# Optimization experiments

Measured on AMD Instinct MI355X. Metric: run time of the kernel, lower is better.

Reference implementation:

```python
import jax, jax.numpy as jnp
import numpy as np

N_NODES = 50000
NEG_SLOPE = 0.2


def _gat_layer(x, src, dst, W, att_src, att_dst, bias, concat):
    # x: [N, F_in]; W: [F_in, H*D]; att_*: [H, D]; bias: [H*D] or [D]
    H, D = att_src.shape
    N = x.shape[0]
    h = (x @ W).reshape(N, H, D)                       # [N, H, D]
    a_s = jnp.einsum('nhd,hd->nh', h, att_src)         # [N, H]
    a_d = jnp.einsum('nhd,hd->nh', h, att_dst)
    e = a_s[src] + a_d[dst]                            # [E, H]
    e = jnp.where(e > 0, e, NEG_SLOPE * e)             # LeakyReLU(0.2)
    # segment softmax over incoming edges of each target node
    e_max = jax.ops.segment_max(e, dst, num_segments=N)
    ex = jnp.exp(e - e_max[dst])
    denom = jax.ops.segment_sum(ex, dst, num_segments=N)
    alpha = ex / denom[dst]                            # [E, H]
    msg = h[src] * alpha[:, :, None]                   # [E, H, D]
    out = jax.ops.segment_sum(msg, dst, num_segments=N)  # [N, H, D]
    if concat:
        out = out.reshape(N, H * D)
    else:
        out = out.mean(axis=1)
    return out + bias


def _forward(x, edge_index, W1, att_src1, att_dst1, b1, W2, att_src2, att_dst2, b2):
    N = x.shape[0]
    loop = jnp.arange(N, dtype=edge_index.dtype)
    src = jnp.concatenate([edge_index[0], loop])       # add self-loops (PyG default)
    dst = jnp.concatenate([edge_index[1], loop])
    h = _gat_layer(x, src, dst, W1, att_src1, att_dst1, b1, concat=True)
    h = jax.nn.elu(h)
    h = _gat_layer(h, src, dst, W2, att_src2, att_dst2, b2, concat=False)
    return jax.nn.log_softmax(h, axis=-1)


def setup_inputs() -> dict:
    key = jax.random.key(0)
    ks = jax.random.split(key, 12)
    N, E, F_in, F_out, H, D = N_NODES, 1600000, 128, 64, 8, 32
    glorot = lambda k, shp: jax.random.normal(k, shp, jnp.float32) * np.sqrt(2.0 / (shp[0] + shp[-1]))
    return {
        'x': jax.random.normal(ks[0], (N, F_in), jnp.float32),
        'edge_index': jax.random.randint(ks[1], (2, E), 0, N, jnp.int64),
        'W1': glorot(ks[2], (F_in, H * D)),
        'att_src1': glorot(ks[3], (H, D)),
        'att_dst1': glorot(ks[4], (H, D)),
        'b1': jnp.zeros((H * D,), jnp.float32),
        'W2': glorot(ks[5], (H * D, F_out)),
        'att_src2': glorot(ks[6], (1, F_out)),
        'att_dst2': glorot(ks[7], (1, F_out)),
        'b2': jnp.zeros((F_out,), jnp.float32),
    }


def reference(x, edge_index, W1, att_src1, att_dst1, b1, W2, att_src2, att_dst2, b2):
    return _forward(x, edge_index, W1, att_src1, att_dst1, b1, W2, att_src2, att_dst2, b2)
```

## Files before the change

### kernel.cpp

```cpp
#include <hip/hip_runtime.h>
#include <hip/hip_bf16.h>
#include <math.h>


#define FIN 128
#define C1 256
#define NH 8
#define HD 32
#define C2 64
#define CH1 64

typedef float floatx2 __attribute__((ext_vector_type(2)));
typedef short bf16x8 __attribute__((ext_vector_type(8)));
typedef float f32x4 __attribute__((ext_vector_type(4)));

__device__ __forceinline__ float blo(unsigned u) { return __uint_as_float(u << 16); }
__device__ __forceinline__ float bhi(unsigned u) { return __uint_as_float(u & 0xffff0000u); }
__device__ __forceinline__ unsigned pkbf(float a, float b) {
    unsigned ua = __float_as_uint(a), ub = __float_as_uint(b);
    ua += 0x7fff + ((ua >> 16) & 1);
    ub += 0x7fff + ((ub >> 16) & 1);
    return (ua >> 16) | (ub & 0xffff0000u);
}

__global__ void init_kernel(const float* __restrict__ W1, const float* __restrict__ W2,
                            int* __restrict__ cnt, unsigned short* __restrict__ w1t,
                            unsigned short* __restrict__ w2t, int n) {
    int i = blockIdx.x * 256 + threadIdx.x;
    if (i < n) cnt[i] = 1;
    if (i < C1 * FIN) {
        int j = i >> 7, k = i & 127;
        float v = W1[(size_t)k * C1 + j];
        w1t[i] = (unsigned short)(pkbf(v, v) & 0xffffu);
    } else if (i < C1 * FIN + C2 * C1) {
        int j2 = i - C1 * FIN;
        int j = j2 >> 8, k = j2 & 255;
        float v = W2[(size_t)k * C2 + j];
        w2t[j2] = (unsigned short)(pkbf(v, v) & 0xffffu);
    }
}

__global__ void hist_kernel(const int* __restrict__ ei, int E, int T,
                            int* cnt, int* __restrict__ offs) {
    int base = blockIdx.x * 256 + threadIdx.x;
    if (base >= T) return;
    int d[4], o[4];
    #pragma unroll
    for (int i = 0; i < 4; ++i) {
        int e = base + i * T;
        d[i] = (e < E) ? ei[E + e] : -1;
    }
    #pragma unroll
    for (int i = 0; i < 4; ++i)
        if (d[i] >= 0) o[i] = atomicAdd(&cnt[d[i]], 1);
    #pragma unroll
    for (int i = 0; i < 4; ++i)
        if (d[i] >= 0) offs[base + i * T] = o[i];
}

__global__ void scan1_kernel(const int* __restrict__ cnt, int n,
                             int* __restrict__ pref, int* __restrict__ bsum) {
    int tid = threadIdx.x, lane = tid & 63, w = tid >> 6;
    int i = blockIdx.x * 256 + tid;
    int v = (i < n) ? cnt[i] : 0;
    int sc = v;
    #pragma unroll
    for (int d = 1; d < 64; d <<= 1) {
        int t = __shfl_up(sc, d, 64);
        if (lane >= d) sc += t;
    }
    __shared__ int ws[4];
    if (lane == 63) ws[w] = sc;
    __syncthreads();
    int woff = 0;
    #pragma unroll
    for (int k = 0; k < 4; ++k) woff += (k < w) ? ws[k] : 0;
    if (i < n) pref[i] = woff + sc - v;
    if (tid == 255) bsum[blockIdx.x] = woff + sc;
}

__global__ void scan2_kernel(int* bsum, int nb) {
    int tid = threadIdx.x, lane = tid & 63, w = tid >> 6;
    int v = (tid < nb) ? bsum[tid] : 0;
    int sc = v;
    #pragma unroll
    for (int d = 1; d < 64; d <<= 1) {
        int t = __shfl_up(sc, d, 64);
        if (lane >= d) sc += t;
    }
    __shared__ int ws[4];
    if (lane == 63) ws[w] = sc;
    __syncthreads();
    int woff = 0;
    #pragma unroll
    for (int k = 0; k < 4; ++k) woff += (k < w) ? ws[k] : 0;
    __syncthreads();
    if (tid < nb) bsum[tid] = woff + sc - v;
}

__global__ void scan3_kernel(const int* __restrict__ pref, const int* __restrict__ bsum,
                             int n, int ETOT, int* __restrict__ rowptr,
                             int* __restrict__ colb) {
    int i = blockIdx.x * 256 + threadIdx.x;
    if (i < n) {
        int rp = pref[i] + bsum[blockIdx.x];
        rowptr[i] = rp;
        colb[rp] = i;
    }
    if (i == 0) rowptr[n] = ETOT;
}

__global__ __launch_bounds__(256) void gemm1_scatter_fused(
    const float* __restrict__ x, const unsigned short* __restrict__ w1t,
    const float* __restrict__ att_s, const float* __restrict__ att_d,
    unsigned char* __restrict__ h1, float* __restrict__ as1, float* __restrict__ ad1,
    int Nn, int GB1,
    const int* __restrict__ ei, const int* __restrict__ rowptr,
    const int* __restrict__ offs, int E, int T, int* __restrict__ colb) {
    __shared__ __align__(16) unsigned char sA[64 * 256];
    int tid = threadIdx.x;
    if (blockIdx.x >= GB1) {
        int base = (blockIdx.x - GB1) * 256 + tid;
        if (base >= T) return;
        #pragma unroll
        for (int i = 0; i < 4; ++i) {
            int e = base + i * T;
            if (e >= E) continue;
            int src = ei[e], dst = ei[E + e];
            colb[rowptr[dst] + offs[e]] = src;
        }
        return;
    }
    int row0 = blockIdx.x * 64;
    #pragma unroll
    for (int rep = 0; rep < 4; ++rep) {
        int flat = rep * 256 + tid;
        int row = flat >> 4, c16 = flat & 15;
        uint4 v = make_uint4(0u, 0u, 0u, 0u);
        if (row0 + row < Nn) {
            const float4* p = reinterpret_cast<const float4*>(
                x + (size_t)(row0 + row) * FIN + c16 * 8);
            float4 f0 = p[0], f1 = p[1];
            v.x = pkbf(f0.x, f0.y); v.y = pkbf(f0.z, f0.w);
            v.z = pkbf(f1.x, f1.y); v.w = pkbf(f1.z, f1.w);
        }
        *reinterpret_cast<uint4*>(sA + ((row * 256 + c16 * 16) ^ ((row & 7) << 4))) = v;
    }
    __syncthreads();
    int w = tid >> 6, l = tid & 63;
    int lr = l & 15, lq = l >> 4;
    int arow = w * 16 + lr;
    bf16x8 a[4];
    #pragma unroll
    for (int ks = 0; ks < 4; ++ks)
        a[ks] = *reinterpret_cast<const bf16x8*>(
            sA + ((arow * 256 + ks * 64 + lq * 16) ^ ((arow & 7) << 4)));
    const unsigned char* wb = reinterpret_cast<const unsigned char*>(w1t);
    float ps[4] = {0.f, 0.f, 0.f, 0.f}, pd[4] = {0.f, 0.f, 0.f, 0.f};
    #pragma unroll
    for (int nt = 0; nt < 16; ++nt) {
        f32x4 acc = {0.f, 0.f, 0.f, 0.f};
        #pragma unroll
        for (int ks = 0; ks < 4; ++ks) {
            bf16x8 b = *reinterpret_cast<const bf16x8*>(
                wb + (size_t)(nt * 16 + lr) * 256 + ks * 64 + lq * 16);
            acc = __builtin_amdgcn_mfma_f32_16x16x32_bf16(a[ks], b, acc, 0, 0, 0);
        }
        int col = nt * 16 + lr;
        float sa = att_s[col], da = att_d[col];
        #pragma unroll
        for (int reg = 0; reg < 4; ++reg) {
            int row = row0 + w * 16 + lq * 4 + reg;
            if (row < Nn) {
                unsigned pk = __builtin_amdgcn_cvt_pk_fp8_f32(acc[reg], acc[reg], 0, false);
                h1[(size_t)row * C1 + col] = (unsigned char)(pk & 0xffu);
            }
            ps[reg] = fmaf(acc[reg], sa, ps[reg]);
            pd[reg] = fmaf(acc[reg], da, pd[reg]);
        }
        if (nt & 1) {
            #pragma unroll
            for (int reg = 0; reg < 4; ++reg) {
                #pragma unroll
                for (int mk = 8; mk >= 1; mk >>= 1) {
                    ps[reg] += __shfl_xor(ps[reg], mk, 64);
                    pd[reg] += __shfl_xor(pd[reg], mk, 64);
                }
            }
            if (lr == 0) {
                int hh = nt >> 1;
                #pragma unroll
                for (int reg = 0; reg < 4; ++reg) {
                    int row = row0 + w * 16 + lq * 4 + reg;
                    if (row < Nn) {
                        as1[row * NH + hh] = ps[reg];
                        ad1[row * NH + hh] = pd[reg];
                    }
                }
            }
            #pragma unroll
            for (int reg = 0; reg < 4; ++reg) { ps[reg] = 0.f; pd[reg] = 0.f; }
        }
    }
}

__global__ __launch_bounds__(64) void agg1_kernel(
    const int* __restrict__ rowptr, const int* __restrict__ colb,
    const float* __restrict__ as1, const float* __restrict__ ad1,
    const unsigned char* __restrict__ h1, const float* __restrict__ b1,
    __hip_bfloat16* __restrict__ x1e, int N) {
    int lane = threadIdx.x;
    int n = blockIdx.x;
    __shared__ float sp[CH1 * 9];
    __shared__ int soff[CH1];
    __shared__ float advs[NH];
    int start = rowptr[n], end = rowptr[n + 1];
    int h = lane >> 3, sub = lane & 7;
    int half = lane >> 5, l5 = lane & 31;
    int hq = l5 >> 2;
    soff[lane] = 0;
    if (lane < NH) advs[lane] = ad1[n * NH + lane];
    float adr[NH];
    #pragma unroll
    for (int hh = 0; hh < NH; ++hh) adr[hh] = advs[hh];

    float m = -INFINITY, denom = 0.f;
    floatx2 A01 = {0.f, 0.f}, A23 = {0.f, 0.f}, A45 = {0.f, 0.f}, A67 = {0.f, 0.f};
    for (int base = start; base < end; base += CH1) {
        int cn = min(CH1, end - base);
        if (lane < cn) {
            int s = colb[base + lane];
            soff[lane] = s << 8;
            const float4* ap = reinterpret_cast<const float4*>(as1 + (size_t)s * NH);
            float4 q0 = ap[0], q1 = ap[1];
            float av[8] = {q0.x, q0.y, q0.z, q0.w, q1.x, q1.y, q1.z, q1.w};
            #pragma unroll
            for (int hh = 0; hh < NH; ++hh) {
                float e = av[hh] + adr[hh];
                e = e > 0.f ? e : 0.2f * e;
                sp[lane * 9 + hh] = e;
            }
        }
        float cmax = -INFINITY;
        for (int e = sub; e < cn; e += 8) cmax = fmaxf(cmax, sp[e * 9 + h]);
        #pragma unroll
        for (int mk = 4; mk >= 1; mk >>= 1) cmax = fmaxf(cmax, __shfl_xor(cmax, mk, 64));
        float newm = fmaxf(m, cmax);
        float scale = __expf(m - newm);
        float scale_g = __shfl(scale, hq << 3, 64);
        floatx2 s2 = {scale_g, scale_g};
        A01 *= s2; A23 *= s2; A45 *= s2; A67 *= s2;
        denom *= scale; m = newm;
        float psum = 0.f;
        for (int e = sub; e < cn; e += 8) {
            float p = __expf(sp[e * 9 + h] - m);
            sp[e * 9 + h] = p;
            psum += p;
        }
        #pragma unroll
        for (int mk = 4; mk >= 1; mk >>= 1) psum += __shfl_xor(psum, mk, 64);
        denom += psum;
        #pragma unroll 2
        for (int e2 = 0; e2 < cn; e2 += 2) {
            int e = e2 + half;
            bool ok = e < cn;
            int off = soff[ok ? e : 0];
            float p = ok ? sp[e * 9 + hq] : 0.f;
            floatx2 p2 = {p, p};
            uint2 u = *reinterpret_cast<const uint2*>(h1 + off + l5 * 8);
            floatx2 f01 = __builtin_amdgcn_cvt_pk_f32_fp8((int)u.x, false);
            floatx2 f23 = __builtin_amdgcn_cvt_pk_f32_fp8((int)u.x, true);
            floatx2 f45 = __builtin_amdgcn_cvt_pk_f32_fp8((int)u.y, false);
            floatx2 f67 = __builtin_amdgcn_cvt_pk_f32_fp8((int)u.y, true);
            A01 = __builtin_elementwise_fma(p2, f01, A01);
            A23 = __builtin_elementwise_fma(p2, f23, A23);
            A45 = __builtin_elementwise_fma(p2, f45, A45);
            A67 = __builtin_elementwise_fma(p2, f67, A67);
        }
    }
    float a0 = A01.x, a1 = A01.y, a2 = A23.x, a3 = A23.y;
    float a4 = A45.x, a5 = A45.y, a6 = A67.x, a7 = A67.y;
    a0 += __shfl_xor(a0, 32, 64); a1 += __shfl_xor(a1, 32, 64);
    a2 += __shfl_xor(a2, 32, 64); a3 += __shfl_xor(a3, 32, 64);
    a4 += __shfl_xor(a4, 32, 64); a5 += __shfl_xor(a5, 32, 64);
    a6 += __shfl_xor(a6, 32, 64); a7 += __shfl_xor(a7, 32, 64);
    float invd = 1.f / __shfl(denom, hq << 3, 64);
    if (half == 0) {
        const float4* bp = reinterpret_cast<const float4*>(b1 + l5 * 8);
        float4 bv0 = bp[0], bv1 = bp[1];
        float v0 = a0 * invd + bv0.x, v1 = a1 * invd + bv0.y;
        float v2 = a2 * invd + bv0.z, v3 = a3 * invd + bv0.w;
        float v4 = a4 * invd + bv1.x, v5 = a5 * invd + bv1.y;
        float v6 = a6 * invd + bv1.z, v7 = a7 * invd + bv1.w;
        v0 = v0 > 0.f ? v0 : __expf(v0) - 1.f;
        v1 = v1 > 0.f ? v1 : __expf(v1) - 1.f;
        v2 = v2 > 0.f ? v2 : __expf(v2) - 1.f;
        v3 = v3 > 0.f ? v3 : __expf(v3) - 1.f;
        v4 = v4 > 0.f ? v4 : __expf(v4) - 1.f;
        v5 = v5 > 0.f ? v5 : __expf(v5) - 1.f;
        v6 = v6 > 0.f ? v6 : __expf(v6) - 1.f;
        v7 = v7 > 0.f ? v7 : __expf(v7) - 1.f;
        uint4 w;
        w.x = pkbf(v0, v1); w.y = pkbf(v2, v3);
        w.z = pkbf(v4, v5); w.w = pkbf(v6, v7);
        *reinterpret_cast<uint4*>(x1e + (size_t)n * C1 + l5 * 8) = w;
    }
}

__global__ __launch_bounds__(256) void gemm2_mfma(
    const unsigned short* __restrict__ x1e, const unsigned short* __restrict__ w2t,
    const float* __restrict__ att_s2, const float* __restrict__ att_d2,
    unsigned char* __restrict__ h2, float* __restrict__ as2, float* __restrict__ ad2, int Nn) {
    __shared__ __align__(16) unsigned char sA[64 * 512];
    int tid = threadIdx.x;
    int row0 = blockIdx.x * 64;
    #pragma unroll
    for (int rep = 0; rep < 8; ++rep) {
        int flat = rep * 256 + tid;
        int row = flat >> 5, c16 = flat & 31;
        uint4 v = make_uint4(0u, 0u, 0u, 0u);
        if (row0 + row < Nn)
            v = *reinterpret_cast<const uint4*>(
                reinterpret_cast<const unsigned char*>(x1e) + (size_t)(row0 + row) * 512 + c16 * 16);
        *reinterpret_cast<uint4*>(sA + ((row * 512 + c16 * 16) ^ ((row & 7) << 4))) = v;
    }
    __syncthreads();
    int w = tid >> 6, l = tid & 63;
    int lr = l & 15, lq = l >> 4;
    int arow = w * 16 + lr;
    bf16x8 a[8];
    #pragma unroll
    for (int ks = 0; ks < 8; ++ks)
        a[ks] = *reinterpret_cast<const bf16x8*>(
            sA + ((arow * 512 + ks * 64 + lq * 16) ^ ((arow & 7) << 4)));
    const unsigned char* wb = reinterpret_cast<const unsigned char*>(w2t);
    float ps[4] = {0.f, 0.f, 0.f, 0.f}, pd[4] = {0.f, 0.f, 0.f, 0.f};
    #pragma unroll
    for (int nt = 0; nt < 4; ++nt) {
        f32x4 acc = {0.f, 0.f, 0.f, 0.f};
        #pragma unroll
        for (int ks = 0; ks < 8; ++ks) {
            bf16x8 b = *reinterpret_cast<const bf16x8*>(
                wb + (size_t)(nt * 16 + lr) * 512 + ks * 64 + lq * 16);
            acc = __builtin_amdgcn_mfma_f32_16x16x32_bf16(a[ks], b, acc, 0, 0, 0);
        }
        int col = nt * 16 + lr;
        float sa = att_s2[col], da = att_d2[col];
        #pragma unroll
        for (int reg = 0; reg < 4; ++reg) {
            int row = row0 + w * 16 + lq * 4 + reg;
            if (row < Nn) {
                unsigned pk = __builtin_amdgcn_cvt_pk_fp8_f32(acc[reg], acc[reg], 0, false);
                h2[(size_t)row * C2 + col] = (unsigned char)(pk & 0xffu);
            }
            ps[reg] = fmaf(acc[reg], sa, ps[reg]);
            pd[reg] = fmaf(acc[reg], da, pd[reg]);
        }
    }
    #pragma unroll
    for (int reg = 0; reg < 4; ++reg) {
        #pragma unroll
        for (int mk = 8; mk >= 1; mk >>= 1) {
            ps[reg] += __shfl_xor(ps[reg], mk, 64);
            pd[reg] += __shfl_xor(pd[reg], mk, 64);
        }
    }
    if (lr == 0) {
        #pragma unroll
        for (int reg = 0; reg < 4; ++reg) {
            int row = row0 + w * 16 + lq * 4 + reg;
            if (row < Nn) { as2[row] = ps[reg]; ad2[row] = pd[reg]; }
        }
    }
}

__global__ __launch_bounds__(64) void agg2_kernel(
    const int* __restrict__ rowptr, const int* __restrict__ colb,
    const float* __restrict__ as2, const float* __restrict__ ad2,
    const unsigned char* __restrict__ h2, const float* __restrict__ b2,
    float* __restrict__ out, int N) {
    int lane = threadIdx.x;
    int n = blockIdx.x;
    __shared__ float sp2[64];
    __shared__ int soff2[64];
    int start = rowptr[n], end = rowptr[n + 1];
    int q = lane >> 4, l4 = lane & 15;
    soff2[lane] = 0;
    float adn = ad2[n];
    float m = -INFINITY, denom = 0.f;
    floatx2 A01 = {0.f, 0.f}, A23 = {0.f, 0.f};
    for (int base = start; base < end; base += 64) {
        int cn = min(64, end - base);
        float logit = -INFINITY;
        if (lane < cn) {
            int s = colb[base + lane];
            soff2[lane] = s << 6;
            float e = as2[s] + adn;
            logit = e > 0.f ? e : 0.2f * e;
        }
        float cmax = logit;
        #pragma unroll
        for (int mk = 32; mk >= 1; mk >>= 1) cmax = fmaxf(cmax, __shfl_xor(cmax, mk, 64));
        float newm = fmaxf(m, cmax);
        float scale = __expf(m - newm);
        floatx2 s2 = {scale, scale};
        A01 *= s2; A23 *= s2;
        denom *= scale; m = newm;
        float p = (lane < cn) ? __expf(logit - m) : 0.f;
        sp2[lane] = p;
        float psum = p;
        #pragma unroll
        for (int mk = 32; mk >= 1; mk >>= 1) psum += __shfl_xor(psum, mk, 64);
        denom += psum;
        #pragma unroll 2
        for (int e2 = 0; e2 < cn; e2 += 4) {
            int e = e2 + q;
            bool ok = e < cn;
            int off = soff2[ok ? e : 0];
            float pe = ok ? sp2[e] : 0.f;
            floatx2 p2 = {pe, pe};
            unsigned u = *reinterpret_cast<const unsigned*>(h2 + off + l4 * 4);
            floatx2 f01 = __builtin_amdgcn_cvt_pk_f32_fp8((int)u, false);
            floatx2 f23 = __builtin_amdgcn_cvt_pk_f32_fp8((int)u, true);
            A01 = __builtin_elementwise_fma(p2, f01, A01);
            A23 = __builtin_elementwise_fma(p2, f23, A23);
        }
    }
    float a0 = A01.x, a1 = A01.y, a2 = A23.x, a3 = A23.y;
    a0 += __shfl_xor(a0, 16, 64); a1 += __shfl_xor(a1, 16, 64);
    a2 += __shfl_xor(a2, 16, 64); a3 += __shfl_xor(a3, 16, 64);
    a0 += __shfl_xor(a0, 32, 64); a1 += __shfl_xor(a1, 32, 64);
    a2 += __shfl_xor(a2, 32, 64); a3 += __shfl_xor(a3, 32, 64);
    float invd = 1.f / denom;
    const float4* bp = reinterpret_cast<const float4*>(b2 + l4 * 4);
    float4 bv = bp[0];
    float v0 = a0 * invd + bv.x, v1 = a1 * invd + bv.y;
    float v2 = a2 * invd + bv.z, v3 = a3 * invd + bv.w;
    float mx = fmaxf(fmaxf(v0, v1), fmaxf(v2, v3));
    #pragma unroll
    for (int mk = 8; mk >= 1; mk >>= 1) mx = fmaxf(mx, __shfl_xor(mx, mk, 64));
    float sum = __expf(v0 - mx) + __expf(v1 - mx) + __expf(v2 - mx) + __expf(v3 - mx);
    #pragma unroll
    for (int mk = 8; mk >= 1; mk >>= 1) sum += __shfl_xor(sum, mk, 64);
    float ls = logf(sum);
    if (q == 0) {
        float4 o = make_float4(v0 - mx - ls, v1 - mx - ls, v2 - mx - ls, v3 - mx - ls);
        *reinterpret_cast<float4*>(out + (size_t)n * C2 + l4 * 4) = o;
    }
}

extern "C" void kernel_launch(void* const* d_in, const int* in_sizes, int n_in,
                              void* d_out, int out_size, void* d_ws, size_t ws_size,
                              hipStream_t stream) {
    const float* x      = (const float*)d_in[0];
    const int*   ei     = (const int*)d_in[1];
    const float* W1     = (const float*)d_in[2];
    const float* att_s1 = (const float*)d_in[3];
    const float* att_d1 = (const float*)d_in[4];
    const float* b1     = (const float*)d_in[5];
    const float* W2     = (const float*)d_in[6];
    const float* att_s2 = (const float*)d_in[7];
    const float* att_d2 = (const float*)d_in[8];
    const float* b2     = (const float*)d_in[9];
    float* out = (float*)d_out;

    const int N = out_size / C2;
    const int E = in_sizes[1] / 2;
    const int ETOT = E + N;
    const int NB = (N + 255) / 256;

    char* ws = (char*)d_ws;
    size_t off = 0;
    auto alloc = [&](size_t bytes) -> void* {
        void* p = ws + off;
        off += (bytes + 255) & ~(size_t)255;
        return p;
    };
    unsigned char* h1 = (unsigned char*)alloc((size_t)N * C1);
    __hip_bfloat16* x1e = (__hip_bfloat16*)alloc((size_t)N * C1 * 2);
    unsigned short* w1t = (unsigned short*)alloc((size_t)C1 * FIN * 2);
    unsigned short* w2t = (unsigned short*)alloc((size_t)C2 * C1 * 2);
    float* as1  = (float*)alloc((size_t)N * NH * 4);
    float* ad1  = (float*)alloc((size_t)N * NH * 4);
    float* as2  = (float*)alloc((size_t)N * 4);
    float* ad2  = (float*)alloc((size_t)N * 4);
    int*   cnt    = (int*)alloc((size_t)N * 4);
    int*   rowptr = (int*)alloc((size_t)(N + 1) * 4);
    int*   pref   = (int*)alloc((size_t)N * 4);
    int*   bsum   = (int*)alloc((size_t)NB * 4);
    int*   offs   = (int*)alloc((size_t)E * 4);
    int*   colb   = (int*)alloc((size_t)ETOT * 4);
    unsigned char* h2 = h1;

    const int T = (E + 3) / 4;
    init_kernel<<<(N + 255) / 256, 256, 0, stream>>>(W1, W2, cnt, w1t, w2t, N);
    hist_kernel<<<(T + 255) / 256, 256, 0, stream>>>(ei, E, T, cnt, offs);
    scan1_kernel<<<NB, 256, 0, stream>>>(cnt, N, pref, bsum);
    scan2_kernel<<<1, 256, 0, stream>>>(bsum, NB);
    scan3_kernel<<<NB, 256, 0, stream>>>(pref, bsum, N, ETOT, rowptr, colb);

    const int GB1 = (N + 63) / 64;
    const int GSC = (T + 255) / 256;
    gemm1_scatter_fused<<<GB1 + GSC, 256, 0, stream>>>(
        x, w1t, att_s1, att_d1, h1, as1, ad1, N, GB1, ei, rowptr, offs, E, T, colb);

    agg1_kernel<<<N, 64, 0, stream>>>(rowptr, colb, as1, ad1, h1, b1, x1e, N);

    gemm2_mfma<<<(N + 63) / 64, 256, 0, stream>>>((const unsigned short*)x1e, w2t,
                                                  att_s2, att_d2, h2, as2, ad2, N);
    agg2_kernel<<<N, 64, 0, stream>>>(rowptr, colb, as2, ad2, h2, b2, out, N);
}
```

Baseline: 258.3 us.

## Replicate degree histogram counters across eight copies to reduce atomic contention

The in-degree histogram used to build CSR is split into eight replicated counter arrays, with each hist block choosing a replica by its block index. The scan pass builds per-replica prefix offsets and computes per-replica row bases so the scatter pass can place each edge correctly. This targets contention on the global atomics. In exchange it adds eight times the counter memory, extra reads and writes in the scan kernels, and a larger init grid; with random destinations, contention may already be low.

```diff
diff --git a/kernel.cpp b/kernel.cpp
--- a/kernel.cpp
+++ b/kernel.cpp
@@ -9,6 +9,7 @@
 #define HD 32
 #define C2 64
 #define CH1 64
+#define NREP 8
 
 typedef float floatx2 __attribute__((ext_vector_type(2)));
 typedef short bf16x8 __attribute__((ext_vector_type(8)));
@@ -24,10 +25,10 @@
 }
 
 __global__ void init_kernel(const float* __restrict__ W1, const float* __restrict__ W2,
-                            int* __restrict__ cnt, unsigned short* __restrict__ w1t,
+                            int* __restrict__ cnt_r, unsigned short* __restrict__ w1t,
                             unsigned short* __restrict__ w2t, int n) {
     int i = blockIdx.x * 256 + threadIdx.x;
-    if (i < n) cnt[i] = 1;
+    if (i < NREP * n) cnt_r[i] = (i < n) ? 1 : 0;
     if (i < C1 * FIN) {
         int j = i >> 7, k = i & 127;
         float v = W1[(size_t)k * C1 + j];
@@ -40,10 +41,11 @@
     }
 }
 
-__global__ void hist_kernel(const int* __restrict__ ei, int E, int T,
-                            int* cnt, int* __restrict__ offs) {
+__global__ void hist_kernel(const int* __restrict__ ei, int E, int T, int n,
+                            int* cnt_r, int* __restrict__ offs) {
     int base = blockIdx.x * 256 + threadIdx.x;
     if (base >= T) return;
+    int* cnt = cnt_r + (size_t)(blockIdx.x & (NREP - 1)) * n;
     int d[4], o[4];
     #pragma unroll
     for (int i = 0; i < 4; ++i) {
@@ -58,11 +60,19 @@
         if (d[i] >= 0) offs[base + i * T] = o[i];
 }
 
-__global__ void scan1_kernel(const int* __restrict__ cnt, int n,
+__global__ void scan1_kernel(const int* __restrict__ cnt_r, int n,
+                             int* __restrict__ pxr,
                              int* __restrict__ pref, int* __restrict__ bsum) {
     int tid = threadIdx.x, lane = tid & 63, w = tid >> 6;
     int i = blockIdx.x * 256 + tid;
-    int v = (i < n) ? cnt[i] : 0;
+    int v = 0;
+    if (i < n) {
+        #pragma unroll
+        for (int r = 0; r < NREP; ++r) {
+            pxr[(size_t)r * n + i] = v;
+            v += cnt_r[(size_t)r * n + i];
+        }
+    }
     int sc = v;
     #pragma unroll
     for (int d = 1; d < 64; d <<= 1) {
@@ -99,13 +109,17 @@
 }
 
 __global__ void scan3_kernel(const int* __restrict__ pref, const int* __restrict__ bsum,
-                             int n, int ETOT, int* __restrict__ rowptr,
+                             const int* __restrict__ pxr, int n, int ETOT,
+                             int* __restrict__ rowptr, int* __restrict__ rowbase,
                              int* __restrict__ colb) {
     int i = blockIdx.x * 256 + threadIdx.x;
     if (i < n) {
         int rp = pref[i] + bsum[blockIdx.x];
         rowptr[i] = rp;
         colb[rp] = i;
+        #pragma unroll
+        for (int r = 0; r < NREP; ++r)
+            rowbase[(size_t)r * n + i] = rp + pxr[(size_t)r * n + i];
     }
     if (i == 0) rowptr[n] = ETOT;
 }
@@ -115,19 +129,20 @@
     const float* __restrict__ att_s, const float* __restrict__ att_d,
     unsigned char* __restrict__ h1, float* __restrict__ as1, float* __restrict__ ad1,
     int Nn, int GB1,
-    const int* __restrict__ ei, const int* __restrict__ rowptr,
+    const int* __restrict__ ei, const int* __restrict__ rowbase,
     const int* __restrict__ offs, int E, int T, int* __restrict__ colb) {
     __shared__ __align__(16) unsigned char sA[64 * 256];
     int tid = threadIdx.x;
     if (blockIdx.x >= GB1) {
         int base = (blockIdx.x - GB1) * 256 + tid;
         if (base >= T) return;
+        const int* rb = rowbase + (size_t)((base >> 8) & (NREP - 1)) * Nn;
         #pragma unroll
         for (int i = 0; i < 4; ++i) {
             int e = base + i * T;
             if (e >= E) continue;
             int src = ei[e], dst = ei[E + e];
-            colb[rowptr[dst] + offs[e]] = src;
+            colb[rb[dst] + offs[e]] = src;
         }
         return;
     }
@@ -484,25 +499,30 @@
     float* ad1  = (float*)alloc((size_t)N * NH * 4);
     float* as2  = (float*)alloc((size_t)N * 4);
     float* ad2  = (float*)alloc((size_t)N * 4);
-    int*   cnt    = (int*)alloc((size_t)N * 4);
-    int*   rowptr = (int*)alloc((size_t)(N + 1) * 4);
-    int*   pref   = (int*)alloc((size_t)N * 4);
-    int*   bsum   = (int*)alloc((size_t)NB * 4);
-    int*   offs   = (int*)alloc((size_t)E * 4);
-    int*   colb   = (int*)alloc((size_t)ETOT * 4);
+    int*   cnt_r   = (int*)alloc((size_t)NREP * N * 4);
+    int*   pxr     = (int*)alloc((size_t)NREP * N * 4);
+    int*   rowbase = (int*)alloc((size_t)NREP * N * 4);
+    int*   rowptr  = (int*)alloc((size_t)(N + 1) * 4);
+    int*   pref    = (int*)alloc((size_t)N * 4);
+    int*   bsum    = (int*)alloc((size_t)NB * 4);
+    int*   offs    = (int*)alloc((size_t)E * 4);
+    int*   colb    = (int*)alloc((size_t)ETOT * 4);
     unsigned char* h2 = h1;
 
+    int init_total = NREP * N;
+    init_kernel<<<(init_total + 255) / 256, 256, 0, stream>>>(W1, W2, cnt_r, w1t, w2t, N);
+
     const int T = (E + 3) / 4;
-    init_kernel<<<(N + 255) / 256, 256, 0, stream>>>(W1, W2, cnt, w1t, w2t, N);
-    hist_kernel<<<(T + 255) / 256, 256, 0, stream>>>(ei, E, T, cnt, offs);
-    scan1_kernel<<<NB, 256, 0, stream>>>(cnt, N, pref, bsum);
+    hist_kernel<<<(T + 255) / 256, 256, 0, stream>>>(ei, E, T, N, cnt_r, offs);
+
+    scan1_kernel<<<NB, 256, 0, stream>>>(cnt_r, N, pxr, pref, bsum);
     scan2_kernel<<<1, 256, 0, stream>>>(bsum, NB);
-    scan3_kernel<<<NB, 256, 0, stream>>>(pref, bsum, N, ETOT, rowptr, colb);
+    scan3_kernel<<<NB, 256, 0, stream>>>(pref, bsum, pxr, N, ETOT, rowptr, rowbase, colb);
 
     const int GB1 = (N + 63) / 64;
     const int GSC = (T + 255) / 256;
     gemm1_scatter_fused<<<GB1 + GSC, 256, 0, stream>>>(
-        x, w1t, att_s1, att_d1, h1, as1, ad1, N, GB1, ei, rowptr, offs, E, T, colb);
+        x, w1t, att_s1, att_d1, h1, as1, ad1, N, GB1, ei, rowbase, offs, E, T, colb);
 
     agg1_kernel<<<N, 64, 0, stream>>>(rowptr, colb, as1, ad1, h1, b1, x1e, N);
 
```

Measured after the change: 252.9 us. -2.1%, faster.
